# Performance work log

Hardware: AMD Instinct MI355X
Metric: run time of the kernel (lower is better)

Reference implementation:

```python
import jax, jax.numpy as jnp
import numpy as np

T, B, D, H = 512, 128, 256, 256


def setup_inputs() -> dict:
    key = jax.random.key(0)
    k1, k2, k3, k4 = jax.random.split(key, 4)
    X = jax.random.normal(k1, (T, B, D), dtype=jnp.float32)
    h = jnp.zeros((B, H), dtype=jnp.float32)
    # Linear weights, torch layout: weight [out, in], fi has no bias, fh has bias
    Wi = jax.random.normal(k2, (H, D), dtype=jnp.float32) * (1.0 / np.sqrt(D))
    Wh = jax.random.normal(k3, (H, H), dtype=jnp.float32) * (1.0 / np.sqrt(H))
    bh = jax.random.normal(k4, (H,), dtype=jnp.float32) * (1.0 / np.sqrt(H))
    return {"X": X, "h": h, "Wi": Wi, "Wh": Wh, "bh": bh, "many_to_many": 1}


def reference(X, h, Wi, Wh, bh, many_to_many):
    # Elman step: h_{t+1} = sigmoid(x_t @ Wi^T + h_t @ Wh^T + bh)
    def step(h_prev, x_t):
        h_new = jax.nn.sigmoid(x_t @ Wi.T + h_prev @ Wh.T + bh)
        return h_new, h_new

    h_last, hiddens = jax.lax.scan(step, h, X)  # hiddens: [T, B, H]
    if many_to_many:
        return hiddens
    return h_last
```

## Files before the change

kernel.cpp:

```cpp
#include <hip/hip_runtime.h>

#define NT 512
#define NB 128
#define ND 256
#define NH 256

typedef _Float16 h2 __attribute__((ext_vector_type(2)));

#if __has_builtin(__builtin_amdgcn_fdot2)
#define DOT2(a, b, c) __builtin_amdgcn_fdot2((a), (b), (c), false)
#else
#define DOT2(a, b, c) (fmaf((float)(a).x, (float)(b).x, \
                        fmaf((float)(a).y, (float)(b).y, (c))))
#endif

__global__ __launch_bounds__(256) void zprep_kernel(
    const float* __restrict__ X, const float* __restrict__ Wi,
    const float* __restrict__ bh, float* __restrict__ Z)
{
    __shared__ float xsT[64][68];
    __shared__ float wsT[64][68];
    const int tid = threadIdx.x;
    const int tm  = tid & 15, tj = tid >> 4;
    const int m0  = blockIdx.x * 64;
    const int j0  = blockIdx.y * 64;
    const int sm  = tid >> 2, kq = tid & 3;

    float acc[4][4] = {};

    for (int c = 0; c < 4; ++c) {
        const int k0 = c * 64;
        const float* xr = X  + (size_t)(m0 + sm) * ND + k0 + kq * 16;
        const float* wr = Wi + (size_t)(j0 + sm) * ND + k0 + kq * 16;
        #pragma unroll
        for (int i = 0; i < 4; ++i) {
            const float4 xv = *(const float4*)(xr + i * 4);
            const float4 wv = *(const float4*)(wr + i * 4);
            const int kk = kq * 16 + i * 4;
            xsT[kk + 0][sm] = xv.x; xsT[kk + 1][sm] = xv.y;
            xsT[kk + 2][sm] = xv.z; xsT[kk + 3][sm] = xv.w;
            wsT[kk + 0][sm] = wv.x; wsT[kk + 1][sm] = wv.y;
            wsT[kk + 2][sm] = wv.z; wsT[kk + 3][sm] = wv.w;
        }
        __syncthreads();

        #pragma unroll 8
        for (int k = 0; k < 64; ++k) {
            const float4 x4 = *(const float4*)&xsT[k][tm * 4];
            const float4 w4 = *(const float4*)&wsT[k][tj * 4];
            acc[0][0] = fmaf(x4.x, w4.x, acc[0][0]);
            acc[0][1] = fmaf(x4.x, w4.y, acc[0][1]);
            acc[0][2] = fmaf(x4.x, w4.z, acc[0][2]);
            acc[0][3] = fmaf(x4.x, w4.w, acc[0][3]);
            acc[1][0] = fmaf(x4.y, w4.x, acc[1][0]);
            acc[1][1] = fmaf(x4.y, w4.y, acc[1][1]);
            acc[1][2] = fmaf(x4.y, w4.z, acc[1][2]);
            acc[1][3] = fmaf(x4.y, w4.w, acc[1][3]);
            acc[2][0] = fmaf(x4.z, w4.x, acc[2][0]);
            acc[2][1] = fmaf(x4.z, w4.y, acc[2][1]);
            acc[2][2] = fmaf(x4.z, w4.z, acc[2][2]);
            acc[2][3] = fmaf(x4.z, w4.w, acc[2][3]);
            acc[3][0] = fmaf(x4.w, w4.x, acc[3][0]);
            acc[3][1] = fmaf(x4.w, w4.y, acc[3][1]);
            acc[3][2] = fmaf(x4.w, w4.z, acc[3][2]);
            acc[3][3] = fmaf(x4.w, w4.w, acc[3][3]);
        }
        __syncthreads();
    }

    const float4 b4 = *(const float4*)&bh[j0 + tj * 4];
    #pragma unroll
    for (int r = 0; r < 4; ++r) {
        float4 o;
        o.x = acc[r][0] + b4.x; o.y = acc[r][1] + b4.y;
        o.z = acc[r][2] + b4.z; o.w = acc[r][3] + b4.w;
        *(float4*)&Z[(size_t)(m0 + tm * 4 + r) * NH + j0 + tj * 4] = o;
    }
}

__global__ __launch_bounds__(512, 2) void rnn_step_kernel(
    float* __restrict__ ZO,
    const float* __restrict__ h0,
    const float* __restrict__ Wh)
{
    __shared__ h2 hb[2][4 * 36];
    const int b   = blockIdx.x;
    const int tid = threadIdx.x;
    const int ks  = tid & 3;
    const int jb  = tid >> 2;
    const int j0  = jb * 2;

    h2 w0p[32], w1p[32];
    {
        const float* r0 = Wh + (size_t)j0 * NH + ks * 64;
        const float* r1 = r0 + NH;
        #pragma unroll
        for (int i = 0; i < 16; ++i) {
            const float4 a = *(const float4*)(r0 + 4 * i);
            const float4 c = *(const float4*)(r1 + 4 * i);
            w0p[2*i+0] = h2{(_Float16)a.x, (_Float16)a.y};
            w0p[2*i+1] = h2{(_Float16)a.z, (_Float16)a.w};
            w1p[2*i+0] = h2{(_Float16)c.x, (_Float16)c.y};
            w1p[2*i+1] = h2{(_Float16)c.z, (_Float16)c.w};
        }
    }
    #pragma unroll
    for (int i = 0; i < 32; ++i) {
        asm volatile("" : "+v"(reinterpret_cast<unsigned int&>(w0p[i])));
        asm volatile("" : "+v"(reinterpret_cast<unsigned int&>(w1p[i])));
    }

    if (tid < 128) {
        const float2 hp = *(const float2*)(h0 + (size_t)b * NH + tid * 2);
        hb[0][(tid >> 5) * 36 + (tid & 31)] =
            h2{(_Float16)hp.x, (_Float16)hp.y};
    }

    float2 z2 = *(const float2*)(ZO + (size_t)b * NH + j0);
    __syncthreads();

    int cur = 0;
    for (int t = 0; t < NT; ++t) {
        h2 hh[32];
        const h2* hv = &hb[cur][ks * 36];
        #pragma unroll
        for (int i = 0; i < 8; ++i)
            *(float4*)&hh[4 * i] = *(const float4*)&hv[4 * i];

        float a0 = 0.f, a1 = 0.f, c0 = 0.f, c1 = 0.f;
        #pragma unroll
        for (int i = 0; i < 16; ++i) {
            a0 = DOT2(w0p[i],      hh[i],      a0);
            a1 = DOT2(w1p[i],      hh[i],      a1);
            c0 = DOT2(w0p[i + 16], hh[i + 16], c0);
            c1 = DOT2(w1p[i + 16], hh[i + 16], c1);
        }
        float s0 = a0 + c0;
        float s1 = a1 + c1;

        float2 z2n = z2;
        if (t + 1 < NT)
            z2n = *(const float2*)(ZO + ((size_t)(t + 1) * NB + b) * NH + j0);

        s0 += __shfl_xor(s0, 1); s1 += __shfl_xor(s1, 1);
        s0 += __shfl_xor(s0, 2); s1 += __shfl_xor(s1, 2);

        if (ks == 0) {
            const float p0 = z2.x + s0;
            const float p1 = z2.y + s1;
            const float hn0 = 1.0f / (1.0f + __expf(-p0));
            const float hn1 = 1.0f / (1.0f + __expf(-p1));
            hb[cur ^ 1][(jb >> 5) * 36 + (jb & 31)] =
                h2{(_Float16)hn0, (_Float16)hn1};
            *(float2*)(ZO + ((size_t)t * NB + b) * NH + j0) =
                make_float2(hn0, hn1);
        }
        z2 = z2n;
        __syncthreads();
        cur ^= 1;
    }
}

extern "C" void kernel_launch(void* const* d_in, const int* in_sizes, int n_in,
                              void* d_out, int out_size, void* d_ws, size_t ws_size,
                              hipStream_t stream) {
    const float* X  = (const float*)d_in[0];
    const float* h0 = (const float*)d_in[1];
    const float* Wi = (const float*)d_in[2];
    const float* Wh = (const float*)d_in[3];
    const float* bh = (const float*)d_in[4];
    float* out = (float*)d_out;

    dim3 zgrid((NT * NB) / 64, NH / 64);
    zprep_kernel<<<zgrid, 256, 0, stream>>>(X, Wi, bh, out);
    rnn_step_kernel<<<NB, 512, 0, stream>>>(out, h0, Wh);
}
```

Baseline: 428.0 us.

## Process two batch rows per block in recurrent step kernel to reuse weights

Each recurrent block now handles two batch rows, so the register-resident fp16 weights are reused across both rows. This doubles the dot-product work per step per block and halves the grid to 64 blocks. The next-step Z prefetch moves ahead of the compute. The asm barriers that pinned weights in VGPRs are removed, which risks register spills or rematerialisation. Fewer blocks on a many-CU GPU reduce parallelism, and each serial step becomes longer.

```diff
diff --git a/kernel.cpp b/kernel.cpp
--- a/kernel.cpp
+++ b/kernel.cpp
@@ -10,8 +10,8 @@
 #if __has_builtin(__builtin_amdgcn_fdot2)
 #define DOT2(a, b, c) __builtin_amdgcn_fdot2((a), (b), (c), false)
 #else
-#define DOT2(a, b, c) (fmaf((float)(a).x, (float)(b).x, \
-                        fmaf((float)(a).y, (float)(b).y, (c))))
+#define DOT2(a, b, c) (fmaf((float)(a)[0], (float)(b)[0], \
+                        fmaf((float)(a)[1], (float)(b)[1], (c))))
 #endif
 
 __global__ __launch_bounds__(256) void zprep_kernel(
@@ -83,8 +83,8 @@
     const float* __restrict__ h0,
     const float* __restrict__ Wh)
 {
-    __shared__ h2 hb[2][4 * 36];
-    const int b   = blockIdx.x;
+    __shared__ h2 hb[2][2][4 * 36];
+    const int b0  = blockIdx.x * 2;
     const int tid = threadIdx.x;
     const int ks  = tid & 3;
     const int jb  = tid >> 2;
@@ -104,58 +104,73 @@
             w1p[2*i+1] = h2{(_Float16)c.z, (_Float16)c.w};
         }
     }
-    #pragma unroll
-    for (int i = 0; i < 32; ++i) {
-        asm volatile("" : "+v"(reinterpret_cast<unsigned int&>(w0p[i])));
-        asm volatile("" : "+v"(reinterpret_cast<unsigned int&>(w1p[i])));
-    }
 
-    if (tid < 128) {
-        const float2 hp = *(const float2*)(h0 + (size_t)b * NH + tid * 2);
-        hb[0][(tid >> 5) * 36 + (tid & 31)] =
+    if (tid < 256) {
+        const int r = tid >> 7, i = tid & 127;
+        const float2 hp = *(const float2*)(h0 + (size_t)(b0 + r) * NH + i * 2);
+        hb[0][r][(i >> 5) * 36 + (i & 31)] =
             h2{(_Float16)hp.x, (_Float16)hp.y};
     }
 
-    float2 z2 = *(const float2*)(ZO + (size_t)b * NH + j0);
+    float2 zA = *(const float2*)(ZO + (size_t)(b0 + 0) * NH + j0);
+    float2 zB = *(const float2*)(ZO + (size_t)(b0 + 1) * NH + j0);
     __syncthreads();
 
     int cur = 0;
     for (int t = 0; t < NT; ++t) {
-        h2 hh[32];
-        const h2* hv = &hb[cur][ks * 36];
+        h2 hA[32], hB[32];
+        const h2* pA = &hb[cur][0][ks * 36];
+        const h2* pB = &hb[cur][1][ks * 36];
         #pragma unroll
-        for (int i = 0; i < 8; ++i)
-            *(float4*)&hh[4 * i] = *(const float4*)&hv[4 * i];
+        for (int i = 0; i < 8; ++i) {
+            *(float4*)&hA[4 * i] = *(const float4*)&pA[4 * i];
+            *(float4*)&hB[4 * i] = *(const float4*)&pB[4 * i];
+        }
 
-        float a0 = 0.f, a1 = 0.f, c0 = 0.f, c1 = 0.f;
+        float2 zAn = zA, zBn = zB;
+        if (t + 1 < NT) {
+            zAn = *(const float2*)(ZO + ((size_t)(t+1) * NB + b0 + 0) * NH + j0);
+            zBn = *(const float2*)(ZO + ((size_t)(t+1) * NB + b0 + 1) * NH + j0);
+        }
+
+        float a0A = 0.f, a1A = 0.f, a0B = 0.f, a1B = 0.f;
+        float c0A = 0.f, c1A = 0.f, c0B = 0.f, c1B = 0.f;
         #pragma unroll
         for (int i = 0; i < 16; ++i) {
-            a0 = DOT2(w0p[i],      hh[i],      a0);
-            a1 = DOT2(w1p[i],      hh[i],      a1);
-            c0 = DOT2(w0p[i + 16], hh[i + 16], c0);
-            c1 = DOT2(w1p[i + 16], hh[i + 16], c1);
+            a0A = DOT2(w0p[i],      hA[i],      a0A);
+            a0B = DOT2(w0p[i],      hB[i],      a0B);
+            a1A = DOT2(w1p[i],      hA[i],      a1A);
+            a1B = DOT2(w1p[i],      hB[i],      a1B);
+            c0A = DOT2(w0p[i + 16], hA[i + 16], c0A);
+            c0B = DOT2(w0p[i + 16], hB[i + 16], c0B);
+            c1A = DOT2(w1p[i + 16], hA[i + 16], c1A);
+            c1B = DOT2(w1p[i + 16], hB[i + 16], c1B);
         }
-        float s0 = a0 + c0;
-        float s1 = a1 + c1;
+        float s0A = a0A + c0A, s1A = a1A + c1A;
+        float s0B = a0B + c0B, s1B = a1B + c1B;
 
-        float2 z2n = z2;
-        if (t + 1 < NT)
-            z2n = *(const float2*)(ZO + ((size_t)(t + 1) * NB + b) * NH + j0);
-
-        s0 += __shfl_xor(s0, 1); s1 += __shfl_xor(s1, 1);
-        s0 += __shfl_xor(s0, 2); s1 += __shfl_xor(s1, 2);
+        s0A += __shfl_xor(s0A, 1); s1A += __shfl_xor(s1A, 1);
+        s0B += __shfl_xor(s0B, 1); s1B += __shfl_xor(s1B, 1);
+        s0A += __shfl_xor(s0A, 2); s1A += __shfl_xor(s1A, 2);
+        s0B += __shfl_xor(s0B, 2); s1B += __shfl_xor(s1B, 2);
 
         if (ks == 0) {
-            const float p0 = z2.x + s0;
-            const float p1 = z2.y + s1;
-            const float hn0 = 1.0f / (1.0f + __expf(-p0));
-            const float hn1 = 1.0f / (1.0f + __expf(-p1));
-            hb[cur ^ 1][(jb >> 5) * 36 + (jb & 31)] =
-                h2{(_Float16)hn0, (_Float16)hn1};
-            *(float2*)(ZO + ((size_t)t * NB + b) * NH + j0) =
-                make_float2(hn0, hn1);
+            const float p0 = zA.x + s0A, p1 = zA.y + s1A;
+            const float q0 = zB.x + s0B, q1 = zB.y + s1B;
+            const float hA0 = 1.0f / (1.0f + __expf(-p0));
+            const float hA1 = 1.0f / (1.0f + __expf(-p1));
+            const float hB0 = 1.0f / (1.0f + __expf(-q0));
+            const float hB1 = 1.0f / (1.0f + __expf(-q1));
+            hb[cur ^ 1][0][(jb >> 5) * 36 + (jb & 31)] =
+                h2{(_Float16)hA0, (_Float16)hA1};
+            hb[cur ^ 1][1][(jb >> 5) * 36 + (jb & 31)] =
+                h2{(_Float16)hB0, (_Float16)hB1};
+            *(float2*)(ZO + ((size_t)t * NB + b0 + 0) * NH + j0) =
+                make_float2(hA0, hA1);
+            *(float2*)(ZO + ((size_t)t * NB + b0 + 1) * NH + j0) =
+                make_float2(hB0, hB1);
         }
-        z2 = z2n;
+        zA = zAn; zB = zBn;
         __syncthreads();
         cur ^= 1;
     }
@@ -173,5 +188,5 @@
 
     dim3 zgrid((NT * NB) / 64, NH / 64);
     zprep_kernel<<<zgrid, 256, 0, stream>>>(X, Wi, bh, out);
-    rnn_step_kernel<<<NB, 512, 0, stream>>>(out, h0, Wh);
+    rnn_step_kernel<<<NB / 2, 512, 0, stream>>>(out, h0, Wh);
 }
```

After: 657.7 us. +53.7%, slower.

## Use MFMA for recurrent step with 16 batch rows per block

Applied to the files above, without the earlier changes.

Replaces the per-batch-row fdot2 recurrent kernel with one that processes 16 batch rows per block using 16x16x16 fp16 MFMA, keeping Wh fragments resident in registers loaded via inline assembly. Hidden state is staged in padded LDS as the MFMA A operand, and the next step's input projection is prefetched into the accumulator init. This aims to cut per-step arithmetic latency, at the cost of launching only 8 blocks and thus using few compute units.

```diff
diff --git a/kernel.cpp b/kernel.cpp
--- a/kernel.cpp
+++ b/kernel.cpp
@@ -5,14 +5,13 @@
 #define ND 256
 #define NH 256
 
-typedef _Float16 h2 __attribute__((ext_vector_type(2)));
-
-#if __has_builtin(__builtin_amdgcn_fdot2)
-#define DOT2(a, b, c) __builtin_amdgcn_fdot2((a), (b), (c), false)
-#else
-#define DOT2(a, b, c) (fmaf((float)(a).x, (float)(b).x, \
-                        fmaf((float)(a).y, (float)(b).y, (c))))
-#endif
+typedef _Float16 half4v __attribute__((ext_vector_type(4)));
+typedef float f32x4 __attribute__((ext_vector_type(4)));
+typedef float f4 __attribute__((ext_vector_type(4)));
+typedef unsigned int u4 __attribute__((ext_vector_type(4)));
+
+#define MFMA16(a, b, c) \
+    __builtin_amdgcn_mfma_f32_16x16x16f16((a), (b), (c), 0, 0, 0)
 
 __global__ __launch_bounds__(256) void zprep_kernel(
     const float* __restrict__ X, const float* __restrict__ Wi,
@@ -78,84 +77,153 @@
     }
 }
 
-__global__ __launch_bounds__(512, 2) void rnn_step_kernel(
+#define HP 264
+
+#define CVT4(dst, q) do {                         \
+    const f4 f_ = __builtin_bit_cast(f4, (q));    \
+    (dst)[0] = (_Float16)f_[0];                   \
+    (dst)[1] = (_Float16)f_[1];                   \
+    (dst)[2] = (_Float16)f_[2];                   \
+    (dst)[3] = (_Float16)f_[3];                   \
+} while (0)
+
+#define PIN4(x) do {                                   \
+    double d_ = __builtin_bit_cast(double, (x));       \
+    asm volatile("" : "+v"(d_));                       \
+    (x) = __builtin_bit_cast(half4v, d_);              \
+} while (0)
+
+#define LOAD_BASE(wfA, base) do {                                         \
+    u4 q0,q1,q2,q3,q4,q5,q6,q7,q8,q9,q10,q11,q12,q13,q14,q15;             \
+    asm volatile(                                                         \
+        "global_load_dwordx4 %0, %16, off offset:0\n\t"                   \
+        "global_load_dwordx4 %1, %16, off offset:64\n\t"                  \
+        "global_load_dwordx4 %2, %16, off offset:128\n\t"                 \
+        "global_load_dwordx4 %3, %16, off offset:192\n\t"                 \
+        "global_load_dwordx4 %4, %16, off offset:256\n\t"                 \
+        "global_load_dwordx4 %5, %16, off offset:320\n\t"                 \
+        "global_load_dwordx4 %6, %16, off offset:384\n\t"                 \
+        "global_load_dwordx4 %7, %16, off offset:448\n\t"                 \
+        "global_load_dwordx4 %8, %16, off offset:512\n\t"                 \
+        "global_load_dwordx4 %9, %16, off offset:576\n\t"                 \
+        "global_load_dwordx4 %10, %16, off offset:640\n\t"                \
+        "global_load_dwordx4 %11, %16, off offset:704\n\t"                \
+        "global_load_dwordx4 %12, %16, off offset:768\n\t"                \
+        "global_load_dwordx4 %13, %16, off offset:832\n\t"                \
+        "global_load_dwordx4 %14, %16, off offset:896\n\t"                \
+        "global_load_dwordx4 %15, %16, off offset:960\n\t"                \
+        "s_waitcnt vmcnt(0)"                                              \
+        : "=&v"(q0),"=&v"(q1),"=&v"(q2),"=&v"(q3),"=&v"(q4),"=&v"(q5),    \
+          "=&v"(q6),"=&v"(q7),"=&v"(q8),"=&v"(q9),"=&v"(q10),"=&v"(q11),  \
+          "=&v"(q12),"=&v"(q13),"=&v"(q14),"=&v"(q15)                     \
+        : "v"(base));                                                     \
+    CVT4(wfA[0], q0);   CVT4(wfA[1], q1);   CVT4(wfA[2], q2);             \
+    CVT4(wfA[3], q3);   CVT4(wfA[4], q4);   CVT4(wfA[5], q5);             \
+    CVT4(wfA[6], q6);   CVT4(wfA[7], q7);   CVT4(wfA[8], q8);             \
+    CVT4(wfA[9], q9);   CVT4(wfA[10], q10); CVT4(wfA[11], q11);           \
+    CVT4(wfA[12], q12); CVT4(wfA[13], q13); CVT4(wfA[14], q14);           \
+    CVT4(wfA[15], q15);                                                   \
+} while (0)
+
+__global__ __launch_bounds__(256, 1) void rnn_step_kernel(
     float* __restrict__ ZO,
     const float* __restrict__ h0,
     const float* __restrict__ Wh)
 {
-    __shared__ h2 hb[2][4 * 36];
-    const int b   = blockIdx.x;
+    __shared__ _Float16 hl[2][16 * HP];
     const int tid = threadIdx.x;
-    const int ks  = tid & 3;
-    const int jb  = tid >> 2;
-    const int j0  = jb * 2;
-
-    h2 w0p[32], w1p[32];
+    const int b0  = blockIdx.x * 16;
+    const int w4  = (tid >> 6) * 4;
+    const int l   = tid & 63;
+    const int ln  = l & 15;
+    const int lg  = l >> 4;
+
+    half4v wf0[16], wf1[16], wf2[16], wf3[16];
     {
-        const float* r0 = Wh + (size_t)j0 * NH + ks * 64;
-        const float* r1 = r0 + NH;
-        #pragma unroll
-        for (int i = 0; i < 16; ++i) {
-            const float4 a = *(const float4*)(r0 + 4 * i);
-            const float4 c = *(const float4*)(r1 + 4 * i);
-            w0p[2*i+0] = h2{(_Float16)a.x, (_Float16)a.y};
-            w0p[2*i+1] = h2{(_Float16)a.z, (_Float16)a.w};
-            w1p[2*i+0] = h2{(_Float16)c.x, (_Float16)c.y};
-            w1p[2*i+1] = h2{(_Float16)c.z, (_Float16)c.w};
-        }
+        const size_t lgo = (size_t)lg * 4;
+        const unsigned long long bA =
+            (unsigned long long)(Wh + (size_t)((w4 + 0) * 16 + ln) * NH + lgo);
+        const unsigned long long bB =
+            (unsigned long long)(Wh + (size_t)((w4 + 1) * 16 + ln) * NH + lgo);
+        const unsigned long long bC =
+            (unsigned long long)(Wh + (size_t)((w4 + 2) * 16 + ln) * NH + lgo);
+        const unsigned long long bD =
+            (unsigned long long)(Wh + (size_t)((w4 + 3) * 16 + ln) * NH + lgo);
+        LOAD_BASE(wf0, bA);
+        LOAD_BASE(wf1, bB);
+        LOAD_BASE(wf2, bC);
+        LOAD_BASE(wf3, bD);
     }
     #pragma unroll
-    for (int i = 0; i < 32; ++i) {
-        asm volatile("" : "+v"(reinterpret_cast<unsigned int&>(w0p[i])));
-        asm volatile("" : "+v"(reinterpret_cast<unsigned int&>(w1p[i])));
-    }
-
-    if (tid < 128) {
-        const float2 hp = *(const float2*)(h0 + (size_t)b * NH + tid * 2);
-        hb[0][(tid >> 5) * 36 + (tid & 31)] =
-            h2{(_Float16)hp.x, (_Float16)hp.y};
-    }
-
-    float2 z2 = *(const float2*)(ZO + (size_t)b * NH + j0);
+    for (int i = 0; i < 16; ++i) {
+        PIN4(wf0[i]); PIN4(wf1[i]); PIN4(wf2[i]); PIN4(wf3[i]);
+    }
+
+    {
+        const int m  = tid >> 4;
+        const int c0 = (tid & 15) * 16;
+        const float* hp = h0 + (size_t)(b0 + m) * NH + c0;
+        #pragma unroll
+        for (int j = 0; j < 16; ++j)
+            hl[0][m * HP + c0 + j] = (_Float16)hp[j];
+    }
+
+    f32x4 zf0, zf1, zf2, zf3;
+    {
+        const float* zp = ZO + ((size_t)0 * NB + b0 + lg * 4) * NH;
+        const int n0 = (w4 + 0) * 16 + ln, n1 = (w4 + 1) * 16 + ln;
+        const int n2 = (w4 + 2) * 16 + ln, n3 = (w4 + 3) * 16 + ln;
+        zf0[0]=zp[n0]; zf0[1]=zp[NH+n0]; zf0[2]=zp[2*NH+n0]; zf0[3]=zp[3*NH+n0];
+        zf1[0]=zp[n1]; zf1[1]=zp[NH+n1]; zf1[2]=zp[2*NH+n1]; zf1[3]=zp[3*NH+n1];
+        zf2[0]=zp[n2]; zf2[1]=zp[NH+n2]; zf2[2]=zp[2*NH+n2]; zf2[3]=zp[3*NH+n2];
+        zf3[0]=zp[n3]; zf3[1]=zp[NH+n3]; zf3[2]=zp[2*NH+n3]; zf3[3]=zp[3*NH+n3];
+    }
     __syncthreads();
 
     int cur = 0;
     for (int t = 0; t < NT; ++t) {
-        h2 hh[32];
-        const h2* hv = &hb[cur][ks * 36];
-        #pragma unroll
-        for (int i = 0; i < 8; ++i)
-            *(float4*)&hh[4 * i] = *(const float4*)&hv[4 * i];
-
-        float a0 = 0.f, a1 = 0.f, c0 = 0.f, c1 = 0.f;
-        #pragma unroll
-        for (int i = 0; i < 16; ++i) {
-            a0 = DOT2(w0p[i],      hh[i],      a0);
-            a1 = DOT2(w1p[i],      hh[i],      a1);
-            c0 = DOT2(w0p[i + 16], hh[i + 16], c0);
-            c1 = DOT2(w1p[i + 16], hh[i + 16], c1);
-        }
-        float s0 = a0 + c0;
-        float s1 = a1 + c1;
-
-        float2 z2n = z2;
-        if (t + 1 < NT)
-            z2n = *(const float2*)(ZO + ((size_t)(t + 1) * NB + b) * NH + j0);
-
-        s0 += __shfl_xor(s0, 1); s1 += __shfl_xor(s1, 1);
-        s0 += __shfl_xor(s0, 2); s1 += __shfl_xor(s1, 2);
-
-        if (ks == 0) {
-            const float p0 = z2.x + s0;
-            const float p1 = z2.y + s1;
-            const float hn0 = 1.0f / (1.0f + __expf(-p0));
-            const float hn1 = 1.0f / (1.0f + __expf(-p1));
-            hb[cur ^ 1][(jb >> 5) * 36 + (jb & 31)] =
-                h2{(_Float16)hn0, (_Float16)hn1};
-            *(float2*)(ZO + ((size_t)t * NB + b) * NH + j0) =
-                make_float2(hn0, hn1);
-        }
-        z2 = z2n;
+        half4v af[16];
+        #pragma unroll
+        for (int kt = 0; kt < 16; ++kt)
+            af[kt] = *(const half4v*)&hl[cur][ln * HP + kt * 16 + lg * 4];
+
+        f32x4 acc0 = zf0, acc1 = zf1, acc2 = zf2, acc3 = zf3;
+        {
+            const int tn = (t + 1 < NT) ? t + 1 : t;
+            const float* zp = ZO + ((size_t)tn * NB + b0 + lg * 4) * NH;
+            const int n0 = (w4 + 0) * 16 + ln, n1 = (w4 + 1) * 16 + ln;
+            const int n2 = (w4 + 2) * 16 + ln, n3 = (w4 + 3) * 16 + ln;
+            zf0[0]=zp[n0]; zf0[1]=zp[NH+n0]; zf0[2]=zp[2*NH+n0]; zf0[3]=zp[3*NH+n0];
+            zf1[0]=zp[n1]; zf1[1]=zp[NH+n1]; zf1[2]=zp[2*NH+n1]; zf1[3]=zp[3*NH+n1];
+            zf2[0]=zp[n2]; zf2[1]=zp[NH+n2]; zf2[2]=zp[2*NH+n2]; zf2[3]=zp[3*NH+n2];
+            zf3[0]=zp[n3]; zf3[1]=zp[NH+n3]; zf3[2]=zp[2*NH+n3]; zf3[3]=zp[3*NH+n3];
+        }
+
+        #pragma unroll
+        for (int kt = 0; kt < 16; ++kt) {
+            acc0 = MFMA16(af[kt], wf0[kt], acc0);
+            acc1 = MFMA16(af[kt], wf1[kt], acc1);
+            acc2 = MFMA16(af[kt], wf2[kt], acc2);
+            acc3 = MFMA16(af[kt], wf3[kt], acc3);
+        }
+
+        {
+            float* op = ZO + ((size_t)t * NB + b0 + lg * 4) * NH;
+            _Float16* lp = &hl[cur ^ 1][(lg * 4) * HP];
+            #define FIN(accX, NT2) do {                                     \
+                const int n_ = (w4 + NT2) * 16 + ln;                        \
+                const float v0_ = 1.0f / (1.0f + __expf(-(accX)[0]));       \
+                const float v1_ = 1.0f / (1.0f + __expf(-(accX)[1]));       \
+                const float v2_ = 1.0f / (1.0f + __expf(-(accX)[2]));       \
+                const float v3_ = 1.0f / (1.0f + __expf(-(accX)[3]));       \
+                op[n_] = v0_;          op[NH + n_] = v1_;                   \
+                op[2 * NH + n_] = v2_; op[3 * NH + n_] = v3_;               \
+                lp[n_] = (_Float16)v0_;          lp[HP + n_] = (_Float16)v1_; \
+                lp[2 * HP + n_] = (_Float16)v2_; lp[3 * HP + n_] = (_Float16)v3_; \
+            } while (0)
+            FIN(acc0, 0); FIN(acc1, 1); FIN(acc2, 2); FIN(acc3, 3);
+            #undef FIN
+        }
         __syncthreads();
         cur ^= 1;
     }
@@ -173,5 +241,5 @@
 
     dim3 zgrid((NT * NB) / 64, NH / 64);
     zprep_kernel<<<zgrid, 256, 0, stream>>>(X, Wi, bh, out);
-    rnn_step_kernel<<<NB, 512, 0, stream>>>(out, h0, Wh);
+    rnn_step_kernel<<<NB / 16, 256, 0, stream>>>(out, h0, Wh);
 }
```

Result: slower. 987.7 us (+130.7%).
